# Kernel tuning notes

Hardware: AMD Instinct MI355X
Metric: run time of the kernel (lower is better)

The kernel has to match this reference:

```python
import jax, jax.numpy as jnp
import numpy as np

N, E = 50000, 800000
IN_DIM, OUT_DIM, HEADS = 128, 256, 8
C = OUT_DIM // HEADS  # per-head channels = 32
NEG_SLOPE = 0.2
LN_EPS = 1e-5


def setup_inputs() -> dict:
    key = jax.random.key(0)
    ks = jax.random.split(key, 8)
    x = jax.random.normal(ks[0], (N, IN_DIM), dtype=jnp.float32)
    edge_index = jax.random.randint(ks[1], (2, E), 0, N, dtype=jnp.int64)
    # GATConv params (glorot-ish scale)
    W = jax.random.normal(ks[2], (IN_DIM, HEADS * C), dtype=jnp.float32) * (1.0 / np.sqrt(IN_DIM))
    att_src = jax.random.normal(ks[3], (HEADS, C), dtype=jnp.float32) * (1.0 / np.sqrt(C))
    att_dst = jax.random.normal(ks[4], (HEADS, C), dtype=jnp.float32) * (1.0 / np.sqrt(C))
    bias = jnp.zeros((OUT_DIM,), dtype=jnp.float32)
    # LayerNorm params
    ln_gamma = jnp.ones((OUT_DIM,), dtype=jnp.float32)
    ln_beta = jnp.zeros((OUT_DIM,), dtype=jnp.float32)
    # Residual Linear (in_dim != out_dim)
    res_W = jax.random.normal(ks[5], (OUT_DIM, IN_DIM), dtype=jnp.float32) * (1.0 / np.sqrt(IN_DIM))
    res_b = jnp.zeros((OUT_DIM,), dtype=jnp.float32)
    return {"x": x, "edge_index": edge_index, "W": W, "att_src": att_src,
            "att_dst": att_dst, "bias": bias, "ln_gamma": ln_gamma,
            "ln_beta": ln_beta, "res_W": res_W, "res_b": res_b}


def reference(x, edge_index, W, att_src, att_dst, bias, ln_gamma, ln_beta, res_W, res_b):
    n = x.shape[0]
    # add self loops (PyG add_self_loops=True)
    loop = jnp.arange(n, dtype=edge_index.dtype)
    src = jnp.concatenate([edge_index[0], loop])
    dst = jnp.concatenate([edge_index[1], loop])

    h = (x @ W).reshape(n, HEADS, C)                      # [N,H,C]
    a_src = jnp.einsum('nhc,hc->nh', h, att_src)          # [N,H]
    a_dst = jnp.einsum('nhc,hc->nh', h, att_dst)

    e = a_src[src] + a_dst[dst]                           # [E+N,H]
    e = jnp.where(e > 0, e, NEG_SLOPE * e)                # LeakyReLU(0.2)

    # segment softmax over destination nodes
    e_max = jax.ops.segment_max(e, dst, num_segments=n)   # [N,H]
    alpha = jnp.exp(e - e_max[dst])
    denom = jax.ops.segment_sum(alpha, dst, num_segments=n)
    alpha = alpha / (denom[dst] + 1e-16)                  # [E+N,H]

    # weighted scatter-add aggregation
    msg = alpha[:, :, None] * h[src]                      # [E+N,H,C]
    out = jax.ops.segment_sum(msg, dst, num_segments=n)   # [N,H,C]
    out = out.reshape(n, HEADS * C) + bias                # concat heads

    # LayerNorm
    mu = out.mean(axis=-1, keepdims=True)
    var = out.var(axis=-1, keepdims=True)
    y = ln_gamma * (out - mu) * jax.lax.rsqrt(var + LN_EPS) + ln_beta

    identity = x @ res_W.T + res_b
    return jax.nn.elu(y + identity)
```

## Files before the change

### kernel.cpp

```cpp
#include <hip/hip_runtime.h>
#include <hip/hip_bf16.h>


typedef __attribute__((ext_vector_type(8))) __bf16 v8bf;
typedef __attribute__((ext_vector_type(4))) float  v4f;

__device__ __forceinline__ float bf2f(unsigned short u) {
    return __uint_as_float(((unsigned int)u) << 16);
}
__device__ __forceinline__ unsigned short f2bf(float f) {
    unsigned int u = __float_as_uint(f);
    u = u + 0x7FFFu + ((u >> 16) & 1u);
    return (unsigned short)(u >> 16);
}

__global__ __launch_bounds__(256) void convert_x_kernel(const float* __restrict__ x,
                                                        unsigned short* __restrict__ xb,
                                                        int total4) {
    int t = blockIdx.x * 256 + threadIdx.x;
    if (t >= total4) return;
    float4 v = *(const float4*)(x + (size_t)t * 4);
    ushort4 o;
    o.x = f2bf(v.x); o.y = f2bf(v.y); o.z = f2bf(v.z); o.w = f2bf(v.w);
    *(ushort4*)(xb + (size_t)t * 4) = o;
}

__global__ __launch_bounds__(256) void pack_Bt_kernel(const float* __restrict__ W,
                                                      const float* __restrict__ resW,
                                                      unsigned short* __restrict__ Bt) {
    int id = blockIdx.x * 256 + threadIdx.x;
    int j = id >> 7;
    int k = id & 127;
    float v = (j < 256) ? W[k * 256 + j] : resW[(size_t)(j - 256) * 128 + k];
    Bt[id] = f2bf(v);
}

__global__ __launch_bounds__(256) void mfma_gemm_kernel(const unsigned short* __restrict__ xb,
                                                        const unsigned short* __restrict__ Bt,
                                                        const float* __restrict__ res_b,
                                                        unsigned short* __restrict__ hb,
                                                        float* __restrict__ iden,
                                                        int N_) {
    __shared__ unsigned short As[64][136];
    __shared__ unsigned short Bs[64][136];
    const int tid = threadIdx.x;
    const int brow = blockIdx.x * 64;
    const int bcol = blockIdx.y * 64;

    #pragma unroll
    for (int it = 0; it < 4; ++it) {
        int cid = it * 256 + tid;
        int row = cid >> 4;
        int c   = cid & 15;
        int grow = brow + row;
        int4 av = make_int4(0, 0, 0, 0);
        if (grow < N_) av = *(const int4*)(xb + (size_t)grow * 128 + c * 8);
        *(int4*)&As[row][c * 8] = av;
        *(int4*)&Bs[row][c * 8] = *(const int4*)(Bt + (size_t)(bcol + row) * 128 + c * 8);
    }
    __syncthreads();

    const int lane = tid & 63;
    const int wid  = tid >> 6;
    const int wm = wid & 1;
    const int wn = wid >> 1;
    const int lm = lane & 15;
    const int lk = lane >> 4;

    v4f acc[2][2] = {};
    #pragma unroll
    for (int ks = 0; ks < 4; ++ks) {
        int koff = ks * 32 + lk * 8;
        v8bf a0 = *(const v8bf*)&As[wm * 32 + lm][koff];
        v8bf a1 = *(const v8bf*)&As[wm * 32 + 16 + lm][koff];
        v8bf b0 = *(const v8bf*)&Bs[wn * 32 + lm][koff];
        v8bf b1 = *(const v8bf*)&Bs[wn * 32 + 16 + lm][koff];
        acc[0][0] = __builtin_amdgcn_mfma_f32_16x16x32_bf16(a0, b0, acc[0][0], 0, 0, 0);
        acc[0][1] = __builtin_amdgcn_mfma_f32_16x16x32_bf16(a0, b1, acc[0][1], 0, 0, 0);
        acc[1][0] = __builtin_amdgcn_mfma_f32_16x16x32_bf16(a1, b0, acc[1][0], 0, 0, 0);
        acc[1][1] = __builtin_amdgcn_mfma_f32_16x16x32_bf16(a1, b1, acc[1][1], 0, 0, 0);
    }

    const bool is_h = (bcol < 256);
    #pragma unroll
    for (int i = 0; i < 2; ++i) {
        #pragma unroll
        for (int j = 0; j < 2; ++j) {
            int col = bcol + wn * 32 + j * 16 + lm;
            float rb = is_h ? 0.f : res_b[col - 256];
            #pragma unroll
            for (int r = 0; r < 4; ++r) {
                int row = brow + wm * 32 + i * 16 + lk * 4 + r;
                if (row >= N_) continue;
                float v = acc[i][j][r];
                if (is_h) hb[(size_t)row * 256 + col] = f2bf(v);
                else      iden[(size_t)row * 256 + (col - 256)] = v + rb;
            }
        }
    }
}

__global__ __launch_bounds__(256) void att_kernel(const unsigned short* __restrict__ hb,
                                                  const float* __restrict__ att_src,
                                                  const float* __restrict__ att_dst,
                                                  float* __restrict__ a_src,
                                                  float* __restrict__ a_dst,
                                                  int N_) {
    int t = blockIdx.x * 256 + threadIdx.x;
    if (t >= N_ * 8) return;
    int hd = t & 7;
    int n  = t >> 3;
    const ushort4* hp = (const ushort4*)(hb + (size_t)n * 256 + hd * 32);
    const float4* as = (const float4*)(att_src + hd * 32);
    const float4* ad = (const float4*)(att_dst + hd * 32);
    float ssum = 0.f, dsum = 0.f;
    #pragma unroll
    for (int i = 0; i < 8; ++i) {
        ushort4 hv = hp[i];
        float h0 = bf2f(hv.x), h1 = bf2f(hv.y), h2 = bf2f(hv.z), h3 = bf2f(hv.w);
        float4 a1 = as[i]; float4 a2 = ad[i];
        ssum += h0 * a1.x + h1 * a1.y + h2 * a1.z + h3 * a1.w;
        dsum += h0 * a2.x + h1 * a2.y + h2 * a2.z + h3 * a2.w;
    }
    a_src[t] = ssum;
    a_dst[t] = dsum;
}

__global__ __launch_bounds__(256) void hist_kernel(const int* __restrict__ ei,
                                                   int* __restrict__ deg, int E_, int N_) {
    int i = blockIdx.x * 256 + threadIdx.x;
    if (i >= E_) return;
    int d = ei[E_ + i];
    if ((unsigned)d < (unsigned)N_) atomicAdd(&deg[d], 1);
}

__global__ __launch_bounds__(256) void scan_part_kernel(const int* __restrict__ deg,
                                                        int* __restrict__ partials,
                                                        int N_) {
    __shared__ int tmp[256];
    int i = blockIdx.x * 256 + threadIdx.x;
    int v = (i < N_) ? deg[i] : 0;
    tmp[threadIdx.x] = v;
    __syncthreads();
    for (int off = 128; off >= 1; off >>= 1) {
        if (threadIdx.x < off) tmp[threadIdx.x] += tmp[threadIdx.x + off];
        __syncthreads();
    }
    if (threadIdx.x == 0) partials[blockIdx.x] = tmp[0];
}

__global__ __launch_bounds__(256) void scan_top_kernel(int* __restrict__ partials, int nparts) {
    __shared__ int tmp[256];
    int t = threadIdx.x;
    int v = (t < nparts) ? partials[t] : 0;
    tmp[t] = v;
    __syncthreads();
    for (int off = 1; off < 256; off <<= 1) {
        int x = (t >= off) ? tmp[t - off] : 0;
        __syncthreads();
        tmp[t] += x;
        __syncthreads();
    }
    if (t < nparts) partials[t] = tmp[t] - v;
}

__global__ __launch_bounds__(256) void scan_final_kernel(int* __restrict__ deg,
                                                         const int* __restrict__ partials,
                                                         int* __restrict__ rowptr,
                                                         int N_) {
    __shared__ int tmp[256];
    int t = threadIdx.x;
    int i = blockIdx.x * 256 + t;
    int v = (i < N_) ? deg[i] : 0;
    tmp[t] = v;
    __syncthreads();
    for (int off = 1; off < 256; off <<= 1) {
        int x = (t >= off) ? tmp[t - off] : 0;
        __syncthreads();
        tmp[t] += x;
        __syncthreads();
    }
    int excl = tmp[t] - v + partials[blockIdx.x];
    if (i < N_) {
        rowptr[i] = excl;
        deg[i] = excl;
        if (i == N_ - 1) rowptr[N_] = excl + v;
    }
}

__global__ __launch_bounds__(256) void scatter_kernel(const int* __restrict__ ei,
                                                      int* __restrict__ cursor,
                                                      int* __restrict__ col,
                                                      int E_, int N_) {
    int i = blockIdx.x * 256 + threadIdx.x;
    if (i >= E_) return;
    int s = ei[i];
    int d = ei[E_ + i];
    if ((unsigned)s >= (unsigned)N_ || (unsigned)d >= (unsigned)N_) return;
    int pos = atomicAdd(&cursor[d], 1);
    col[pos] = s;
}

__global__ __launch_bounds__(256) void gather_finalize_kernel(
        const int* __restrict__ rowptr, const int* __restrict__ col,
        const unsigned short* __restrict__ hb,
        const float* __restrict__ a_src, const float* __restrict__ a_dst,
        const float* __restrict__ bias, const float* __restrict__ gamma,
        const float* __restrict__ beta,
        float* __restrict__ out, int N_) {
    int n = blockIdx.x * 4 + (threadIdx.x >> 6);
    if (n >= N_) return;
    int lane = threadIdx.x & 63;
    int hd = lane >> 3;

    float adst = a_dst[n * 8 + hd];

    float es = a_src[n * 8 + hd] + adst;
    es = es > 0.f ? es : 0.2f * es;
    float w = __expf(es);
    ushort4 hv = *(const ushort4*)(hb + (size_t)n * 256 + lane * 4);
    float accx = w * bf2f(hv.x), accy = w * bf2f(hv.y);
    float accz = w * bf2f(hv.z), accw = w * bf2f(hv.w);
    float wsum = w;

    int beg = rowptr[n], end = rowptr[n + 1];
    for (int e0 = beg; e0 < end; e0 += 64) {
        int myc = (e0 + lane < end) ? col[e0 + lane] : 0;
        int cnt = min(64, end - e0);
        #pragma unroll 4
        for (int j = 0; j < cnt; ++j) {
            int s = __shfl(myc, j);
            float ea = a_src[s * 8 + hd] + adst;
            ea = ea > 0.f ? ea : 0.2f * ea;
            float we = __expf(ea);
            ushort4 hs = *(const ushort4*)(hb + (size_t)s * 256 + lane * 4);
            accx += we * bf2f(hs.x); accy += we * bf2f(hs.y);
            accz += we * bf2f(hs.z); accw += we * bf2f(hs.w);
            wsum += we;
        }
    }

    float inv_w = 1.f / (wsum + 1e-16f);
    float4 b4 = *(const float4*)(bias + lane * 4);
    float v0 = accx * inv_w + b4.x;
    float v1 = accy * inv_w + b4.y;
    float v2 = accz * inv_w + b4.z;
    float v3 = accw * inv_w + b4.w;

    float sum = v0 + v1 + v2 + v3;
    float sumsq = v0 * v0 + v1 * v1 + v2 * v2 + v3 * v3;
    #pragma unroll
    for (int o = 32; o >= 1; o >>= 1) {
        sum   += __shfl_xor(sum, o);
        sumsq += __shfl_xor(sumsq, o);
    }
    float mean = sum * (1.f / 256.f);
    float var  = sumsq * (1.f / 256.f) - mean * mean;
    float inv  = rsqrtf(var + 1e-5f);

    float4 g4  = *(const float4*)(gamma + lane * 4);
    float4 be4 = *(const float4*)(beta + lane * 4);
    float4 id4 = *(const float4*)(out + (size_t)n * 256 + lane * 4);

    float y0 = g4.x * (v0 - mean) * inv + be4.x + id4.x;
    float y1 = g4.y * (v1 - mean) * inv + be4.y + id4.y;
    float y2 = g4.z * (v2 - mean) * inv + be4.z + id4.z;
    float y3 = g4.w * (v3 - mean) * inv + be4.w + id4.w;
    float4 r;
    r.x = y0 > 0.f ? y0 : (__expf(y0) - 1.f);
    r.y = y1 > 0.f ? y1 : (__expf(y1) - 1.f);
    r.z = y2 > 0.f ? y2 : (__expf(y2) - 1.f);
    r.w = y3 > 0.f ? y3 : (__expf(y3) - 1.f);
    *(float4*)(out + (size_t)n * 256 + lane * 4) = r;
}

extern "C" void kernel_launch(void* const* d_in, const int* in_sizes, int n_in,
                              void* d_out, int out_size, void* d_ws, size_t ws_size,
                              hipStream_t stream) {
    const float* x       = (const float*)d_in[0];
    const int*   ei      = (const int*)d_in[1];
    const float* W       = (const float*)d_in[2];
    const float* att_src = (const float*)d_in[3];
    const float* att_dst = (const float*)d_in[4];
    const float* bias    = (const float*)d_in[5];
    const float* gamma   = (const float*)d_in[6];
    const float* beta    = (const float*)d_in[7];
    const float* res_W   = (const float*)d_in[8];
    const float* res_b   = (const float*)d_in[9];
    float* out = (float*)d_out;

    const int N_ = in_sizes[0] / 128;
    const int E_ = in_sizes[1] / 2;

    unsigned short* xb = (unsigned short*)d_ws;
    unsigned short* hb = xb + (size_t)N_ * 128;
    unsigned short* Bt = hb + (size_t)N_ * 256;
    float* a_src  = (float*)(Bt + 512 * 128);
    float* a_dst  = a_src + (size_t)N_ * 8;
    int*   deg    = (int*)(a_dst + (size_t)N_ * 8);
    int*   rowptr = deg + N_;
    int*   parts  = rowptr + N_ + 1;
    int*   col    = parts + 256;

    const int nchunk = (N_ + 255) / 256;

    hipMemsetAsync(deg, 0, (size_t)N_ * sizeof(int), stream);
    hist_kernel<<<(E_ + 255) / 256, 256, 0, stream>>>(ei, deg, E_, N_);
    scan_part_kernel<<<nchunk, 256, 0, stream>>>(deg, parts, N_);
    scan_top_kernel<<<1, 256, 0, stream>>>(parts, nchunk);
    scan_final_kernel<<<nchunk, 256, 0, stream>>>(deg, parts, rowptr, N_);
    scatter_kernel<<<(E_ + 255) / 256, 256, 0, stream>>>(ei, deg, col, E_, N_);

    int total4 = N_ * 128 / 4;
    convert_x_kernel<<<(total4 + 255) / 256, 256, 0, stream>>>(x, xb, total4);
    pack_Bt_kernel<<<256, 256, 0, stream>>>(W, res_W, Bt);
    dim3 ggrid((N_ + 63) / 64, 8);
    mfma_gemm_kernel<<<ggrid, 256, 0, stream>>>(xb, Bt, res_b, hb, out, N_);
    att_kernel<<<(N_ * 8 + 255) / 256, 256, 0, stream>>>(hb, att_src, att_dst, a_src, a_dst, N_);

    gather_finalize_kernel<<<(N_ + 3) / 4, 256, 0, stream>>>(
        rowptr, col, hb, a_src, a_dst, bias, gamma, beta, out, N_);
}
```

Before: 329.9 us.

## Fuse x conversion, GEMM over all columns, and attention logits into one kernel

Drops the separate fp32-to-bf16 conversion kernel and converts x while loading it into shared memory. Each block now keeps its A fragments in registers and loops over all 8 column tiles, so x is read once per row block. The output tile is staged through shared memory so that h can be stored with coalesced vector writes and the per-head attention dot products can be computed there, which removes att_kernel and its re-read of h. The cost is fewer blocks (one per 64 rows instead of 8), a serial column loop with extra barriers, and higher register and shared-memory use per block.

Measured after the change: 308.3 us. 6.5% less time.

```diff
diff --git a/kernel.cpp b/kernel.cpp
--- a/kernel.cpp
+++ b/kernel.cpp
@@ -12,17 +12,6 @@
     unsigned int u = __float_as_uint(f);
     u = u + 0x7FFFu + ((u >> 16) & 1u);
     return (unsigned short)(u >> 16);
-}
-
-__global__ __launch_bounds__(256) void convert_x_kernel(const float* __restrict__ x,
-                                                        unsigned short* __restrict__ xb,
-                                                        int total4) {
-    int t = blockIdx.x * 256 + threadIdx.x;
-    if (t >= total4) return;
-    float4 v = *(const float4*)(x + (size_t)t * 4);
-    ushort4 o;
-    o.x = f2bf(v.x); o.y = f2bf(v.y); o.z = f2bf(v.z); o.w = f2bf(v.w);
-    *(ushort4*)(xb + (size_t)t * 4) = o;
 }
 
 __global__ __launch_bounds__(256) void pack_Bt_kernel(const float* __restrict__ W,
@@ -35,17 +24,21 @@
     Bt[id] = f2bf(v);
 }
 
-__global__ __launch_bounds__(256) void mfma_gemm_kernel(const unsigned short* __restrict__ xb,
+__global__ __launch_bounds__(256) void mfma_gemm_kernel(const float* __restrict__ x,
                                                         const unsigned short* __restrict__ Bt,
+                                                        const float* __restrict__ att_src,
+                                                        const float* __restrict__ att_dst,
                                                         const float* __restrict__ res_b,
                                                         unsigned short* __restrict__ hb,
                                                         float* __restrict__ iden,
+                                                        float* __restrict__ a_src,
+                                                        float* __restrict__ a_dst,
                                                         int N_) {
     __shared__ unsigned short As[64][136];
     __shared__ unsigned short Bs[64][136];
+    __shared__ float Cs[64][68];
     const int tid = threadIdx.x;
     const int brow = blockIdx.x * 64;
-    const int bcol = blockIdx.y * 64;
 
     #pragma unroll
     for (int it = 0; it < 4; ++it) {
@@ -53,12 +46,19 @@
         int row = cid >> 4;
         int c   = cid & 15;
         int grow = brow + row;
-        int4 av = make_int4(0, 0, 0, 0);
-        if (grow < N_) av = *(const int4*)(xb + (size_t)grow * 128 + c * 8);
-        *(int4*)&As[row][c * 8] = av;
-        *(int4*)&Bs[row][c * 8] = *(const int4*)(Bt + (size_t)(bcol + row) * 128 + c * 8);
-    }
-    __syncthreads();
+        unsigned int w[4];
+        if (grow < N_) {
+            const float4* xp = (const float4*)(x + (size_t)grow * 128 + c * 8);
+            float4 v0 = xp[0], v1 = xp[1];
+            w[0] = (unsigned)f2bf(v0.x) | ((unsigned)f2bf(v0.y) << 16);
+            w[1] = (unsigned)f2bf(v0.z) | ((unsigned)f2bf(v0.w) << 16);
+            w[2] = (unsigned)f2bf(v1.x) | ((unsigned)f2bf(v1.y) << 16);
+            w[3] = (unsigned)f2bf(v1.z) | ((unsigned)f2bf(v1.w) << 16);
+        } else {
+            w[0] = w[1] = w[2] = w[3] = 0u;
+        }
+        *(int4*)&As[row][c * 8] = make_int4(w[0], w[1], w[2], w[3]);
+    }
 
     const int lane = tid & 63;
     const int wid  = tid >> 6;
@@ -67,63 +67,102 @@
     const int lm = lane & 15;
     const int lk = lane >> 4;
 
-    v4f acc[2][2] = {};
-    #pragma unroll
-    for (int ks = 0; ks < 4; ++ks) {
-        int koff = ks * 32 + lk * 8;
-        v8bf a0 = *(const v8bf*)&As[wm * 32 + lm][koff];
-        v8bf a1 = *(const v8bf*)&As[wm * 32 + 16 + lm][koff];
-        v8bf b0 = *(const v8bf*)&Bs[wn * 32 + lm][koff];
-        v8bf b1 = *(const v8bf*)&Bs[wn * 32 + 16 + lm][koff];
-        acc[0][0] = __builtin_amdgcn_mfma_f32_16x16x32_bf16(a0, b0, acc[0][0], 0, 0, 0);
-        acc[0][1] = __builtin_amdgcn_mfma_f32_16x16x32_bf16(a0, b1, acc[0][1], 0, 0, 0);
-        acc[1][0] = __builtin_amdgcn_mfma_f32_16x16x32_bf16(a1, b0, acc[1][0], 0, 0, 0);
-        acc[1][1] = __builtin_amdgcn_mfma_f32_16x16x32_bf16(a1, b1, acc[1][1], 0, 0, 0);
-    }
-
-    const bool is_h = (bcol < 256);
-    #pragma unroll
-    for (int i = 0; i < 2; ++i) {
+    const int tRow = tid >> 2;
+    const int tcc  = (tid & 3) * 16;
+
+    v8bf afr[4][2];
+    bool afr_loaded = false;
+
+    #pragma unroll 1
+    for (int bc = 0; bc < 8; ++bc) {
         #pragma unroll
-        for (int j = 0; j < 2; ++j) {
-            int col = bcol + wn * 32 + j * 16 + lm;
-            float rb = is_h ? 0.f : res_b[col - 256];
+        for (int it = 0; it < 4; ++it) {
+            int cid = it * 256 + tid;
+            int row = cid >> 4;
+            int c   = cid & 15;
+            *(int4*)&Bs[row][c * 8] =
+                *(const int4*)(Bt + (size_t)(bc * 64 + row) * 128 + c * 8);
+        }
+        __syncthreads();
+
+        if (!afr_loaded) {
+            afr_loaded = true;
             #pragma unroll
-            for (int r = 0; r < 4; ++r) {
-                int row = brow + wm * 32 + i * 16 + lk * 4 + r;
-                if (row >= N_) continue;
-                float v = acc[i][j][r];
-                if (is_h) hb[(size_t)row * 256 + col] = f2bf(v);
-                else      iden[(size_t)row * 256 + (col - 256)] = v + rb;
+            for (int ks = 0; ks < 4; ++ks) {
+                int koff = ks * 32 + lk * 8;
+                afr[ks][0] = *(const v8bf*)&As[wm * 32 + lm][koff];
+                afr[ks][1] = *(const v8bf*)&As[wm * 32 + 16 + lm][koff];
             }
         }
-    }
-}
-
-__global__ __launch_bounds__(256) void att_kernel(const unsigned short* __restrict__ hb,
-                                                  const float* __restrict__ att_src,
-                                                  const float* __restrict__ att_dst,
-                                                  float* __restrict__ a_src,
-                                                  float* __restrict__ a_dst,
-                                                  int N_) {
-    int t = blockIdx.x * 256 + threadIdx.x;
-    if (t >= N_ * 8) return;
-    int hd = t & 7;
-    int n  = t >> 3;
-    const ushort4* hp = (const ushort4*)(hb + (size_t)n * 256 + hd * 32);
-    const float4* as = (const float4*)(att_src + hd * 32);
-    const float4* ad = (const float4*)(att_dst + hd * 32);
-    float ssum = 0.f, dsum = 0.f;
-    #pragma unroll
-    for (int i = 0; i < 8; ++i) {
-        ushort4 hv = hp[i];
-        float h0 = bf2f(hv.x), h1 = bf2f(hv.y), h2 = bf2f(hv.z), h3 = bf2f(hv.w);
-        float4 a1 = as[i]; float4 a2 = ad[i];
-        ssum += h0 * a1.x + h1 * a1.y + h2 * a1.z + h3 * a1.w;
-        dsum += h0 * a2.x + h1 * a2.y + h2 * a2.z + h3 * a2.w;
-    }
-    a_src[t] = ssum;
-    a_dst[t] = dsum;
+
+        v4f acc[2][2] = {};
+        #pragma unroll
+        for (int ks = 0; ks < 4; ++ks) {
+            int koff = ks * 32 + lk * 8;
+            v8bf b0 = *(const v8bf*)&Bs[wn * 32 + lm][koff];
+            v8bf b1 = *(const v8bf*)&Bs[wn * 32 + 16 + lm][koff];
+            acc[0][0] = __builtin_amdgcn_mfma_f32_16x16x32_bf16(afr[ks][0], b0, acc[0][0], 0, 0, 0);
+            acc[0][1] = __builtin_amdgcn_mfma_f32_16x16x32_bf16(afr[ks][0], b1, acc[0][1], 0, 0, 0);
+            acc[1][0] = __builtin_amdgcn_mfma_f32_16x16x32_bf16(afr[ks][1], b0, acc[1][0], 0, 0, 0);
+            acc[1][1] = __builtin_amdgcn_mfma_f32_16x16x32_bf16(afr[ks][1], b1, acc[1][1], 0, 0, 0);
+        }
+
+        #pragma unroll
+        for (int i = 0; i < 2; ++i)
+            #pragma unroll
+            for (int j = 0; j < 2; ++j)
+                #pragma unroll
+                for (int r = 0; r < 4; ++r)
+                    Cs[wm * 32 + i * 16 + lk * 4 + r][wn * 32 + j * 16 + lm] = acc[i][j][r];
+        __syncthreads();
+
+        int grow = brow + tRow;
+        if (grow < N_) {
+            int gcol = bc * 64 + tcc;
+            float vs[16];
+            #pragma unroll
+            for (int q = 0; q < 4; ++q) {
+                float4 t4 = *(const float4*)&Cs[tRow][tcc + q * 4];
+                vs[q * 4 + 0] = t4.x; vs[q * 4 + 1] = t4.y;
+                vs[q * 4 + 2] = t4.z; vs[q * 4 + 3] = t4.w;
+            }
+            if (gcol < 256) {
+                int head = gcol >> 5;
+                int chb  = gcol & 31;
+                float ps = 0.f, pd = 0.f;
+                #pragma unroll
+                for (int c = 0; c < 16; ++c) {
+                    ps += vs[c] * att_src[head * 32 + chb + c];
+                    pd += vs[c] * att_dst[head * 32 + chb + c];
+                }
+                ps += __shfl_xor(ps, 1);
+                pd += __shfl_xor(pd, 1);
+                if (!(tid & 1)) {
+                    a_src[grow * 8 + head] = ps;
+                    a_dst[grow * 8 + head] = pd;
+                }
+                unsigned int w[8];
+                #pragma unroll
+                for (int c = 0; c < 8; ++c)
+                    w[c] = (unsigned)f2bf(vs[2 * c]) | ((unsigned)f2bf(vs[2 * c + 1]) << 16);
+                unsigned short* hp = hb + (size_t)grow * 256 + gcol;
+                *(int4*)hp       = make_int4(w[0], w[1], w[2], w[3]);
+                *(int4*)(hp + 8) = make_int4(w[4], w[5], w[6], w[7]);
+            } else {
+                int oc = gcol - 256;
+                float* ip = iden + (size_t)grow * 256 + oc;
+                #pragma unroll
+                for (int q = 0; q < 4; ++q) {
+                    float4 v = make_float4(vs[q * 4 + 0], vs[q * 4 + 1],
+                                           vs[q * 4 + 2], vs[q * 4 + 3]);
+                    const float4 rb = *(const float4*)(res_b + oc + q * 4);
+                    v.x += rb.x; v.y += rb.y; v.z += rb.z; v.w += rb.w;
+                    *(float4*)(ip + q * 4) = v;
+                }
+            }
+        }
+        __syncthreads();
+    }
 }
 
 __global__ __launch_bounds__(256) void hist_kernel(const int* __restrict__ ei,
@@ -292,8 +331,7 @@
     const int N_ = in_sizes[0] / 128;
     const int E_ = in_sizes[1] / 2;
 
-    unsigned short* xb = (unsigned short*)d_ws;
-    unsigned short* hb = xb + (size_t)N_ * 128;
+    unsigned short* hb = (unsigned short*)d_ws;
     unsigned short* Bt = hb + (size_t)N_ * 256;
     float* a_src  = (float*)(Bt + 512 * 128);
     float* a_dst  = a_src + (size_t)N_ * 8;
@@ -311,12 +349,9 @@
     scan_final_kernel<<<nchunk, 256, 0, stream>>>(deg, parts, rowptr, N_);
     scatter_kernel<<<(E_ + 255) / 256, 256, 0, stream>>>(ei, deg, col, E_, N_);
 
-    int total4 = N_ * 128 / 4;
-    convert_x_kernel<<<(total4 + 255) / 256, 256, 0, stream>>>(x, xb, total4);
     pack_Bt_kernel<<<256, 256, 0, stream>>>(W, res_W, Bt);
-    dim3 ggrid((N_ + 63) / 64, 8);
-    mfma_gemm_kernel<<<ggrid, 256, 0, stream>>>(xb, Bt, res_b, hb, out, N_);
-    att_kernel<<<(N_ * 8 + 255) / 256, 256, 0, stream>>>(hb, att_src, att_dst, a_src, a_dst, N_);
+    mfma_gemm_kernel<<<(N_ + 63) / 64, 256, 0, stream>>>(
+        x, Bt, att_src, att_dst, res_b, hb, out, a_src, a_dst, N_);
 
     gather_finalize_kernel<<<(N_ + 3) / 4, 256, 0, stream>>>(
         rowptr, col, hb, a_src, a_dst, bias, gamma, beta, out, N_);
```
